# Optimization experiments

Measured on AMD Instinct MI355X. Metric: run time of the kernel, lower is better.

The kernel has to match this reference:

```python
import jax, jax.numpy as jnp
import numpy as np

B, T, HID = 8, 2048, 1024
NH, MD = 16, 16
UFC = 2  # len(use_for_context) = ['lr', 'rl']
MAT_EPS = 1e-5
VEC_EPS = 1e-6
SQRT_MD = float(np.sqrt(MD))


def setup_inputs() -> dict:
    key = jax.random.key(0)
    ks = jax.random.split(key, 5)
    s_in = 1.0 / np.sqrt(HID)
    s_out = 1.0 / np.sqrt(NH * MD * UFC)
    return {
        "hidden_states": jax.random.normal(ks[0], (B, T, HID), jnp.float32),
        "W_mat": jax.random.uniform(ks[1], (HID, NH * MD * MD), jnp.float32, -s_in, s_in),
        "b_mat": jax.random.uniform(ks[2], (NH * MD * MD,), jnp.float32, -s_in, s_in),
        "W_out": jax.random.uniform(ks[3], (NH * MD * UFC, HID), jnp.float32, -s_out, s_out),
        "b_out": jax.random.uniform(ks[4], (HID,), jnp.float32, -s_out, s_out),
    }


def _scan_vectors(m, v0, reverse):
    """Sequential matrix-vector recurrence with per-step L2 normalization.
    m: (T, B*NH, d, d); v0: (B*NH, d). Returns history (T, B*NH, d)
    (equal to torch history[1:] for lr, and reversed(history[1:]) for rl)."""
    def step(v, m_t):
        nv = jnp.einsum('bij,bj->bi', m_t, v)
        nv = nv / (jnp.linalg.norm(nv, axis=-1, keepdims=True) + VEC_EPS)
        return nv, nv
    _, hist = jax.lax.scan(step, v0, m, reverse=reverse)
    return hist


def reference(hidden_states, W_mat, b_mat, W_out, b_out):
    # predict_matrix: fc_to_mat + Frobenius matrix normalization ([-2,-1] branch)
    m = hidden_states @ W_mat + b_mat                       # (B, T, NH*MD*MD)
    m = m.reshape(B, T, NH, MD, MD).transpose(1, 0, 2, 3, 4)  # (T, B, NH, d, d)
    fro = jnp.linalg.norm(m, axis=(-2, -1), keepdims=True)
    m_norm = m / (fro + MAT_EPS) * SQRT_MD
    m_norm = m_norm.reshape(T, B * NH, MD, MD)

    # init_type == 'one': v[..., 0, :] = 1 -> e_0
    v0 = jnp.zeros((B * NH, MD), jnp.float32).at[:, 0].set(1.0)

    v_lr = _scan_vectors(m_norm, v0, reverse=False)  # (T, B*NH, d)
    v_rl = _scan_vectors(m_norm, v0, reverse=True)   # (T, B*NH, d)

    def to_bthd(v):
        return v.reshape(T, B, NH, MD).transpose(1, 0, 2, 3)  # (B, T, NH, d)

    x = jnp.concatenate([to_bthd(v_lr), to_bthd(v_rl)], axis=-1)  # (B, T, NH, 2d)
    # networks_for_heads == 'common': flatten heads, Linear, gelu (exact erf form)
    x = x.reshape(B, T, NH * MD * UFC) @ W_out + b_out
    return jax.nn.gelu(x, approximate=False)
```

## Files before the change

### kernel.cpp

```cpp
#include <hip/hip_runtime.h>
#include <math.h>

#define Tdim 2048
#define HIDd 1024
#define NHd 16
#define NCOL 4096
#define Cn 64
#define Ln 32
#define LSTR 40
#define KCAT 3072
#define KB 6144

typedef _Float16 f16x4  __attribute__((ext_vector_type(4)));
typedef _Float16 f16x8  __attribute__((ext_vector_type(8)));
typedef float    f32x4  __attribute__((ext_vector_type(4)));

typedef __attribute__((address_space(1))) void gvoid_t;
typedef __attribute__((address_space(3))) void lvoid_t;

__global__ __launch_bounds__(256) void conv_A_kernel(const float* __restrict__ hs,
                                                     _Float16* __restrict__ Ac)
{
    const size_t i = ((size_t)blockIdx.x * 256 + threadIdx.x) * 8;
    const size_t r = i >> 10, k = i & 1023;
    const float4 x0 = *(const float4*)(hs + i);
    const float4 x1 = *(const float4*)(hs + i + 4);
    const float v[8] = {x0.x, x0.y, x0.z, x0.w, x1.x, x1.y, x1.z, x1.w};
    f16x8 h, hm, l;
#pragma unroll
    for (int j = 0; j < 8; ++j) {
        const _Float16 hh = (_Float16)v[j];
        h[j]  = hh;
        hm[j] = (_Float16)(v[j] * 0.03125f);
        l[j]  = (_Float16)((v[j] - (float)hh) * 32.0f);
    }
    _Float16* o = Ac + r * KCAT + k;
    *(f16x8*)(o)        = h;
    *(f16x8*)(o + 1024) = hm;
    *(f16x8*)(o + 2048) = l;
}

__global__ __launch_bounds__(256) void conv_B_kernel(const float* __restrict__ W,
                                                     _Float16* __restrict__ Bc)
{
    __shared__ float t[32][33];
    const int tx = threadIdx.x & 31, ty = threadIdx.x >> 5;
    const int n0 = blockIdx.x * 32, k0 = blockIdx.y * 32;
#pragma unroll
    for (int i = 0; i < 4; ++i)
        t[ty + i * 8][tx] = W[(size_t)(k0 + ty + i * 8) * NCOL + n0 + tx];
    __syncthreads();
#pragma unroll
    for (int i = 0; i < 4; ++i) {
        const float w = t[tx][ty + i * 8];
        const _Float16 h = (_Float16)w;
        const size_t o = (size_t)(n0 + ty + i * 8) * KCAT + k0 + tx;
        Bc[o]        = h;
        Bc[o + 1024] = (_Float16)((w - (float)h) * 32.0f);
        Bc[o + 2048] = (_Float16)((float)h * 0.03125f);
    }
}

__global__ __launch_bounds__(256) void conv_W2T_kernel(const float* __restrict__ W,
                                                       _Float16* __restrict__ WT)
{
    __shared__ float t[32][33];
    const int tx = threadIdx.x & 31, ty = threadIdx.x >> 5;
    const int n0 = blockIdx.x * 32, k0 = blockIdx.y * 32;
#pragma unroll
    for (int i = 0; i < 4; ++i)
        t[ty + i * 8][tx] = W[(size_t)(k0 + ty + i * 8) * 1024 + n0 + tx];
    __syncthreads();
#pragma unroll
    for (int i = 0; i < 4; ++i)
        WT[(size_t)(n0 + ty + i * 8) * 512 + k0 + tx] = (_Float16)t[tx][ty + i * 8];
}

#define MFMA_PHASE(CPH) \
    _Pragma("unroll") \
    for (int m2_ = 0; m2_ < 2; ++m2_) { \
        _Pragma("unroll") \
        for (int nt_ = 0; nt_ < 4; ++nt_) { \
            acc[(CPH)*2 + m2_][nt_] = __builtin_amdgcn_mfma_f32_16x16x32_f16(af[m2_][0], bf[nt_][0], acc[(CPH)*2 + m2_][nt_], 0, 0, 0); \
            acc[(CPH)*2 + m2_][nt_] = __builtin_amdgcn_mfma_f32_16x16x32_f16(af[m2_][1], bf[nt_][1], acc[(CPH)*2 + m2_][nt_], 0, 0, 0); \
        } \
    }

#define PHASE(BUF, CPH, STAGE_EXPR, DOGATE) do { \
    af[0][0] = readA(BUF, (CPH)*2,     0); \
    af[0][1] = readA(BUF, (CPH)*2,     1); \
    af[1][0] = readA(BUF, (CPH)*2 + 1, 0); \
    af[1][1] = readA(BUF, (CPH)*2 + 1, 1); \
    if ((CPH) == 0) { \
        _Pragma("unroll") \
        for (int nt_ = 0; nt_ < 4; ++nt_) { bf[nt_][0] = readB(BUF, nt_, 0); bf[nt_][1] = readB(BUF, nt_, 1); } \
    } \
    STAGE_EXPR; \
    asm volatile("s_barrier" ::: "memory"); \
    asm volatile("s_waitcnt lgkmcnt(0)" ::: "memory"); \
    __builtin_amdgcn_sched_barrier(0); \
    __builtin_amdgcn_s_setprio(1); \
    MFMA_PHASE(CPH) \
    __builtin_amdgcn_s_setprio(0); \
    if (DOGATE) { \
        if (notlast) asm volatile("s_waitcnt vmcnt(6)" ::: "memory"); \
        else         asm volatile("s_waitcnt vmcnt(0)" ::: "memory"); \
    } \
    asm volatile("s_barrier" ::: "memory"); \
} while (0)

__global__ __launch_bounds__(512, 2) void gemm1_8ph(const _Float16* __restrict__ A,
                                                    const _Float16* __restrict__ B,
                                                    const float* __restrict__ bias,
                                                    float* __restrict__ Mout,
                                                    float* __restrict__ qout, int SS)
{
    __shared__ __align__(16) _Float16 sAB[4][256 * 64];
    const int tid = threadIdx.x;
    const int lane = tid & 63;
    const int wid = tid >> 6;
    const int wm = wid >> 2, wn = wid & 3;
    const int q = lane >> 4, ln = lane & 15;
    const int col0 = blockIdx.x * 256;
    const int row0 = blockIdx.y * 256;

    const char* Ab = (const char*)A + (size_t)row0 * KB;
    const char* Bb = (const char*)B + (size_t)col0 * KB;

    auto stage_chunk = [&](const char* g, int fr, int kt, char* ldsbase) {
        const int rr = tid >> 3;
        const int cb = (tid & 7) << 4;
        const char* src = g + (size_t)(fr + rr) * KB + (size_t)kt * 128 + (cb ^ ((rr & 7) << 4));
        char* dst = ldsbase + ((tid >> 6) << 10);
        __builtin_amdgcn_global_load_lds((gvoid_t*)src, (lvoid_t*)dst, 16, 0, 0);
    };
    auto stageA2g = [&](int b, int t, int h) {
        stage_chunk(Ab, h * 64,       t, (char*)&sAB[b][0] + (size_t)(h * 64) * 128);
        stage_chunk(Ab, 128 + h * 64, t, (char*)&sAB[b][0] + (size_t)(128 + h * 64) * 128);
    };
    auto stageB2 = [&](int b, int t, int h) {
        stage_chunk(Bb, h * 128,      t, (char*)&sAB[2 + b][0] + (size_t)(h * 128) * 128);
        stage_chunk(Bb, h * 128 + 64, t, (char*)&sAB[2 + b][0] + (size_t)(h * 128 + 64) * 128);
    };
    auto readA = [&](int b, int mf, int ks) -> f16x8 {
        const int r = wm * 128 + mf * 16 + ln;
        return *(const f16x8*)((const char*)&sAB[b][0] + r * 128 + ((ks * 64 + q * 16) ^ ((r & 7) << 4)));
    };
    auto readB = [&](int b, int nt, int ks) -> f16x8 {
        const int r = wn * 64 + nt * 16 + ln;
        return *(const f16x8*)((const char*)&sAB[2 + b][0] + r * 128 + ((ks * 64 + q * 16) ^ ((r & 7) << 4)));
    };

    stageB2(0, 0, 0); stageB2(0, 0, 1); stageA2g(0, 0, 0); stageA2g(0, 0, 1);
    stageB2(1, 1, 0); stageB2(1, 1, 1); stageA2g(1, 1, 0);

    f32x4 acc[8][4];
    const f32x4 z4 = {0.f, 0.f, 0.f, 0.f};
#pragma unroll
    for (int mf = 0; mf < 8; ++mf)
#pragma unroll
        for (int nt = 0; nt < 4; ++nt) acc[mf][nt] = z4;

    asm volatile("s_waitcnt vmcnt(6)" ::: "memory");
    asm volatile("s_barrier" ::: "memory");

    f16x8 af[2][2];
    f16x8 bf[4][2];

#pragma unroll 1
    for (int it = 0; it < 24; ++it) {
        const int t0 = it * 2;
        const bool notlast = (it != 23);
        PHASE(0, 0, (stageA2g(1, t0 + 1, 1)), 0);
        PHASE(0, 1, (notlast ? stageB2(0, t0 + 2, 0) : (void)0), 0);
        PHASE(0, 2, (notlast ? stageB2(0, t0 + 2, 1) : (void)0), 0);
        PHASE(0, 3, (notlast ? stageA2g(0, t0 + 2, 0) : (void)0), 1);
        PHASE(1, 0, (notlast ? stageA2g(0, t0 + 2, 1) : (void)0), 0);
        PHASE(1, 1, (notlast ? stageB2(1, t0 + 3, 0) : (void)0), 0);
        PHASE(1, 2, (notlast ? stageB2(1, t0 + 3, 1) : (void)0), 0);
        PHASE(1, 3, (notlast ? stageA2g(1, t0 + 3, 0) : (void)0), 1);
    }

    float* Mf = (float*)&sAB[0][0];
    const int seq = ((row0 >> 11) << 4) + blockIdx.x;
    const int cc   = wid & 3;
    const int dirw = wid >> 2;
    float bv[4];
#pragma unroll
    for (int nt = 0; nt < 4; ++nt) bv[nt] = bias[col0 + wn * 64 + nt * 16 + ln];

#pragma unroll 1
    for (int half = 0; half < 2; ++half) {
        __syncthreads();
        if (wm == half) {
#pragma unroll
            for (int mf = 0; mf < 8; ++mf)
#pragma unroll
                for (int nt = 0; nt < 4; ++nt)
#pragma unroll
                    for (int r = 0; r < 4; ++r)
                        Mf[(mf * 16 + q * 4 + r) * 256 + wn * 64 + nt * 16 + ln]
                            = acc[mf][nt][r] + bv[nt];
        }
        __syncthreads();

        const int cblk = half * 4 + cc;
        const int tb   = cblk * 32 - half * 128;
        float v[4];
#pragma unroll
        for (int r = 0; r < 4; ++r) v[r] = (q * 4 + r == ln) ? 1.0f : 0.0f;

        int tl = dirw ? (tb + 31) : tb;
        const int ds = dirw ? -1 : 1;
        float4 arow = *(const float4*)&Mf[tl * 256 + ln * 16 + q * 4];
        float f2 = arow.x*arow.x + arow.y*arow.y + arow.z*arow.z + arow.w*arow.w;
#pragma unroll
        for (int off = 1; off < 64; off <<= 1) f2 += __shfl_xor(f2, off);
        float sm = 4.0f * rsqrtf(f2 + 1e-12f);

        for (int s = 0; s < Ln; ++s) {
            const int tabs = (row0 & 2047) + (dirw ? (cblk * 32 + 31 - s) : (cblk * 32 + s));
            f16x4 mh, mlo;
            const float ar[4] = {arow.x * sm, arow.y * sm, arow.z * sm, arow.w * sm};
#pragma unroll
            for (int i = 0; i < 4; ++i) {
                const _Float16 h = (_Float16)ar[i];
                mh[i] = h; mlo[i] = (_Float16)((ar[i] - (float)h) * 1024.0f);
            }
            float smn = sm;
            if (s + 1 < Ln) {
                tl += ds;
                arow = *(const float4*)&Mf[tl * 256 + ln * 16 + q * 4];
                float f2n = arow.x*arow.x + arow.y*arow.y + arow.z*arow.z + arow.w*arow.w;
#pragma unroll
                for (int off = 1; off < 64; off <<= 1) f2n += __shfl_xor(f2n, off);
                smn = 4.0f * rsqrtf(f2n + 1e-12f);
            }
            f16x4 qh, ql;
#pragma unroll
            for (int r = 0; r < 4; ++r) {
                const _Float16 h = (_Float16)v[r];
                qh[r] = h; ql[r] = (_Float16)((v[r] - (float)h) * 1024.0f);
            }
            f32x4 a1 = {0.f,0.f,0.f,0.f}, a2 = {0.f,0.f,0.f,0.f};
            a1 = __builtin_amdgcn_mfma_f32_16x16x16f16(mh,  qh, a1, 0, 0, 0);
            a2 = __builtin_amdgcn_mfma_f32_16x16x16f16(mh,  ql, a2, 0, 0, 0);
            a2 = __builtin_amdgcn_mfma_f32_16x16x16f16(mlo, qh, a2, 0, 0, 0);
#pragma unroll
            for (int r = 0; r < 4; ++r) v[r] = a1[r] + a2[r] * (1.0f / 1024.0f);

            if (s & 1) {
                float mx = 0.f;
#pragma unroll
                for (int r = 0; r < 4; ++r) mx = fmaxf(mx, fabsf(v[r]));
#pragma unroll
                for (int off = 1; off < 64; off <<= 1) mx = fmaxf(mx, __shfl_xor(mx, off));
                const float inv = 1.0f / (mx + 1e-30f);
#pragma unroll
                for (int r = 0; r < 4; ++r) v[r] *= inv;
            }
            _Float16* Pp = (_Float16*)((char*)Mout
                         + ((size_t)seq * Tdim + tabs) * 1024 + dirw * 512);
#pragma unroll
            for (int r = 0; r < 4; ++r)
                Pp[(q * 4 + r) * 16 + ln] = (_Float16)v[r];
            sm = smn;
        }

        float ss = 0.f;
#pragma unroll
        for (int r = 0; r < 4; ++r) ss += v[r] * v[r];
#pragma unroll
        for (int off = 1; off < 64; off <<= 1) ss += __shfl_xor(ss, off);
        const float sl = 1.0f / (sqrtf(ss) + 1e-30f);
        const int cabs = ((row0 & 2047) >> 5) + cblk;
        float* qo = qout + ((size_t)(dirw * SS + seq) * Cn + cabs) * 256;
#pragma unroll
        for (int r = 0; r < 4; ++r)
            qo[(q * 4 + r) * 16 + ln] = v[r] * sl;
    }
}

__global__ __launch_bounds__(64) void stageB_kernel(const float* __restrict__ q,
                                                    float* __restrict__ vs, int SS)
{
    const int lane = threadIdx.x & 63;
    const int i = lane & 15;
    const int chain = blockIdx.x;
    const int dir = (chain >= SS) ? 1 : 0;
    const int seq = chain - dir * SS;
    const float* qb = q + (size_t)(dir * SS + seq) * Cn * 256;
    float* vb = vs + (size_t)(dir * SS + seq) * Cn * 16;

    float myw = (i == 0) ? 1.0f : 0.0f;
    float wv[16];
#pragma unroll
    for (int k2 = 0; k2 < 16; ++k2) wv[k2] = (k2 == 0) ? 1.0f : 0.0f;

    int cc = dir ? (Cn - 1) : 0;
    const float* Qp = qb + (size_t)cc * 256 + i * 16;
    float4 q0 = *(const float4*)(Qp + 0);
    float4 q1 = *(const float4*)(Qp + 4);
    float4 q2 = *(const float4*)(Qp + 8);
    float4 q3 = *(const float4*)(Qp + 12);

    for (int s = 0; s < Cn; ++s) {
        vb[cc * 16 + i] = myw;
        float nv = q0.x*wv[0] + q0.y*wv[1] + q0.z*wv[2] + q0.w*wv[3]
                 + q1.x*wv[4] + q1.y*wv[5] + q1.z*wv[6] + q1.w*wv[7]
                 + q2.x*wv[8] + q2.y*wv[9] + q2.z*wv[10] + q2.w*wv[11]
                 + q3.x*wv[12] + q3.y*wv[13] + q3.z*wv[14] + q3.w*wv[15];
        if (s + 1 < Cn) {
            const int ccn = dir ? (Cn - 2 - s) : (s + 1);
            const float* Qn = qb + (size_t)ccn * 256 + i * 16;
            q0 = *(const float4*)(Qn + 0);
            q1 = *(const float4*)(Qn + 4);
            q2 = *(const float4*)(Qn + 8);
            q3 = *(const float4*)(Qn + 12);
        }
        float s2 = nv * nv;
        s2 += __shfl_xor(s2, 1); s2 += __shfl_xor(s2, 2);
        s2 += __shfl_xor(s2, 4); s2 += __shfl_xor(s2, 8);
        const float wn = nv / (sqrtf(s2) + 1e-20f);
        myw = wn;
#pragma unroll
        for (int k2 = 0; k2 < 16; ++k2) wv[k2] = __shfl(wn, (lane & 48) | k2);
        cc = dir ? (Cn - 2 - s) : (s + 1);
    }
}

__global__ __launch_bounds__(256) void stageC2_kernel(const float* __restrict__ m,
                                                      const float* __restrict__ vs,
                                                      _Float16* __restrict__ x, int SS)
{
    const int tid = threadIdx.x;
    const int wave = tid >> 6, lane = tid & 63;
    const int dsc = blockIdx.x * 4 + wave;
    const int dirseq = dsc >> 6, c = dsc & (Cn - 1);
    const int dir = (dirseq >= SS) ? 1 : 0;
    const int seq = dirseq - dir * SS;
    const int bbl = seq >> 4, h = seq & 15;
    const _Float16* Pp = (const _Float16*)((const char*)m
                       + ((size_t)seq * Tdim + c * Ln) * 1024 + dir * 512);
    const float* vp = vs + (size_t)dsc * 16;

    float v[16];
#pragma unroll
    for (int k = 0; k < 16; ++k) v[k] = vp[k];

    const int tt = lane >> 4, j = lane & 15;
    const int t0 = c * Ln;
#pragma unroll
    for (int g = 0; g < 8; ++g) {
        const int s = g * 4 + tt;
        const _Float16* pr = Pp + (size_t)s * 512 + j * 16;
        const f16x8 p0 = *(const f16x8*)(pr);
        const f16x8 p1 = *(const f16x8*)(pr + 8);
        float nv = 0.f;
#pragma unroll
        for (int k = 0; k < 8; ++k) nv += (float)p0[k] * v[k];
#pragma unroll
        for (int k = 0; k < 8; ++k) nv += (float)p1[k] * v[k + 8];
        float s2 = nv * nv;
        s2 += __shfl_xor(s2, 1); s2 += __shfl_xor(s2, 2);
        s2 += __shfl_xor(s2, 4); s2 += __shfl_xor(s2, 8);
        const float vn = nv / (sqrtf(s2) + 1e-6f);
        const int t = t0 + s;
        x[(((size_t)bbl * Tdim + t) * NHd + h) * 32 + dir * 16 + j] = (_Float16)vn;
    }
}

__global__ __launch_bounds__(256) void gemm2_f16(const _Float16* __restrict__ A,
                                                 const _Float16* __restrict__ BT,
                                                 const float* __restrict__ bias,
                                                 float* __restrict__ out, int row0)
{
    __shared__ _Float16 Al[128 * LSTR];
    __shared__ _Float16 Bl[128 * LSTR];
    const int tid = threadIdx.x;
    const int wave = tid >> 6, lane = tid & 63;
    const int wm = wave & 1, wn = wave >> 1;
    const int qd = lane >> 4, ln = lane & 15;
    const int r0 = blockIdx.y * 128;
    const int c0 = blockIdx.x * 128;

    f32x4 acc[4][4] = {{{0.f,0.f,0.f,0.f}}};

    const int sr = tid >> 2, sc = tid & 3;
    const _Float16* Ag = A  + (size_t)(r0 + sr) * 512 + sc * 8;
    const _Float16* Bg = BT + (size_t)(c0 + sr) * 512 + sc * 8;
    _Float16* Alw = &Al[sr * LSTR + sc * 8];
    _Float16* Blw = &Bl[sr * LSTR + sc * 8];

    for (int k0 = 0; k0 < 512; k0 += 32) {
        const f16x8 a0 = *(const f16x8*)(Ag + k0);
        const f16x8 a1 = *(const f16x8*)(Ag + (size_t)64 * 512 + k0);
        const f16x8 b0 = *(const f16x8*)(Bg + k0);
        const f16x8 b1 = *(const f16x8*)(Bg + (size_t)64 * 512 + k0);
        __syncthreads();
        *(f16x8*)(Alw)             = a0;
        *(f16x8*)(Alw + 64 * LSTR) = a1;
        *(f16x8*)(Blw)             = b0;
        *(f16x8*)(Blw + 64 * LSTR) = b1;
        __syncthreads();
        f16x8 af[4], bfr[4];
#pragma unroll
        for (int mt = 0; mt < 4; ++mt)
            af[mt] = *(const f16x8*)&Al[(wm * 64 + mt * 16 + ln) * LSTR + qd * 8];
#pragma unroll
        for (int nt = 0; nt < 4; ++nt)
            bfr[nt] = *(const f16x8*)&Bl[(wn * 64 + nt * 16 + ln) * LSTR + qd * 8];
#pragma unroll
        for (int mt = 0; mt < 4; ++mt)
#pragma unroll
            for (int nt = 0; nt < 4; ++nt)
                acc[mt][nt] = __builtin_amdgcn_mfma_f32_16x16x32_f16(af[mt], bfr[nt], acc[mt][nt], 0, 0, 0);
    }
#pragma unroll
    for (int nt = 0; nt < 4; ++nt) {
        const int c = c0 + wn * 64 + nt * 16 + ln;
        const float bv = bias[c];
#pragma unroll
        for (int mt = 0; mt < 4; ++mt) {
#pragma unroll
            for (int r = 0; r < 4; ++r) {
                const int row = r0 + wm * 64 + mt * 16 + qd * 4 + r;
                float v = acc[mt][nt][r] + bv;
                v = 0.5f * v * (1.0f + erff(v * 0.70710678118654752f));
                out[(size_t)(row0 + row) * 1024 + c] = v;
            }
        }
    }
}

extern "C" void kernel_launch(void* const* d_in, const int* in_sizes, int n_in,
                              void* d_out, int out_size, void* d_ws, size_t ws_size,
                              hipStream_t stream)
{
    const float* hs    = (const float*)d_in[0];
    const float* W_mat = (const float*)d_in[1];
    const float* b_mat = (const float*)d_in[2];
    const float* W_out = (const float*)d_in[3];
    const float* b_out = (const float*)d_in[4];
    float* out = (float*)d_out;

    const size_t per_bb = (32ull << 20) + (2ull << 20) + (12ull << 20) + (128ull << 10);
    const size_t wbase  = 25ull << 20;
    int nbb = 8;
    while (nbb > 1 && ws_size < wbase + (size_t)nbb * per_bb) nbb >>= 1;

    char* base = (char*)d_ws;
    _Float16* W2T = (_Float16*)base;
    _Float16* Bc  = (_Float16*)(base + (1ull << 20));
    size_t off = wbase;
    float* m  = (float*)(base + off);  off += (size_t)nbb * (32ull << 20);
    float* qx = (float*)(base + off);  off += (size_t)nbb * (2ull << 20);
    _Float16* Ac = (_Float16*)(base + off); off += (size_t)nbb * (12ull << 20);
    float* vs = (float*)(base + off);

    conv_B_kernel<<<dim3(128, 32), 256, 0, stream>>>(W_mat, Bc);
    conv_W2T_kernel<<<dim3(32, 16), 256, 0, stream>>>(W_out, W2T);

    for (int bb0 = 0; bb0 < 8; bb0 += nbb) {
        const int row0 = bb0 * Tdim;
        const int SS = nbb * 16;
        conv_A_kernel<<<nbb * 1024, 256, 0, stream>>>(hs + (size_t)row0 * HIDd, Ac);
        gemm1_8ph<<<dim3(16, nbb * 8), 512, 0, stream>>>(Ac, Bc, b_mat, m, qx, SS);
        stageB_kernel<<<2 * SS, 64, 0, stream>>>(qx, vs, SS);
        stageC2_kernel<<<SS * Cn / 2, 256, 0, stream>>>(m, vs, (_Float16*)qx, SS);
        gemm2_f16<<<dim3(8, nbb * 16), 256, 0, stream>>>((_Float16*)qx, W2T, b_out, out, row0);
    }
}
```

Measured before the change: 786.3 us.

## Replace output GEMM with 8-phase pipelined global_load_lds kernel and swizzle Mf stores

Rewrites the second GEMM as a 256x256-tile, 512-thread kernel that stages A and B directly into LDS with global_load_lds, using XOR-swizzled layouts and a double-buffered phase schedule reused from the first GEMM. This aims to overlap global loads with MFMA work and cut LDS bank conflicts and per-iteration barriers. It also XOR-swizzles the Mf scratch layout in the scan stage to reduce bank conflicts on the row reads. The larger tiles mean fewer blocks (4x8 per batch chunk), which may lower occupancy and wave balance.

```diff
diff --git a/kernel.cpp b/kernel.cpp
--- a/kernel.cpp
+++ b/kernel.cpp
@@ -7,9 +7,9 @@
 #define NCOL 4096
 #define Cn 64
 #define Ln 32
-#define LSTR 40
 #define KCAT 3072
 #define KB 6144
+#define KB2 1024
 
 typedef _Float16 f16x4  __attribute__((ext_vector_type(4)));
 typedef _Float16 f16x8  __attribute__((ext_vector_type(8)));
@@ -198,9 +198,11 @@
 #pragma unroll
                 for (int nt = 0; nt < 4; ++nt)
 #pragma unroll
-                    for (int r = 0; r < 4; ++r)
-                        Mf[(mf * 16 + q * 4 + r) * 256 + wn * 64 + nt * 16 + ln]
-                            = acc[mf][nt][r] + bv[nt];
+                    for (int r = 0; r < 4; ++r) {
+                        const int mrow = mf * 16 + q * 4 + r;
+                        const int mcol = (wn * 64 + nt * 16 + ln) ^ ((mrow & 4) << 2);
+                        Mf[mrow * 256 + mcol] = acc[mf][nt][r] + bv[nt];
+                    }
         }
         __syncthreads();
 
@@ -212,7 +214,7 @@
 
         int tl = dirw ? (tb + 31) : tb;
         const int ds = dirw ? -1 : 1;
-        float4 arow = *(const float4*)&Mf[tl * 256 + ln * 16 + q * 4];
+        float4 arow = *(const float4*)&Mf[tl * 256 + ((ln * 16 + q * 4) ^ ((tl & 4) << 2))];
         float f2 = arow.x*arow.x + arow.y*arow.y + arow.z*arow.z + arow.w*arow.w;
 #pragma unroll
         for (int off = 1; off < 64; off <<= 1) f2 += __shfl_xor(f2, off);
@@ -230,7 +232,7 @@
             float smn = sm;
             if (s + 1 < Ln) {
                 tl += ds;
-                arow = *(const float4*)&Mf[tl * 256 + ln * 16 + q * 4];
+                arow = *(const float4*)&Mf[tl * 256 + ((ln * 16 + q * 4) ^ ((tl & 4) << 2))];
                 float f2n = arow.x*arow.x + arow.y*arow.y + arow.z*arow.z + arow.w*arow.w;
 #pragma unroll
                 for (int off = 1; off < 64; off <<= 1) f2n += __shfl_xor(f2n, off);
@@ -370,64 +372,89 @@
     }
 }
 
-__global__ __launch_bounds__(256) void gemm2_f16(const _Float16* __restrict__ A,
-                                                 const _Float16* __restrict__ BT,
-                                                 const float* __restrict__ bias,
-                                                 float* __restrict__ out, int row0)
-{
-    __shared__ _Float16 Al[128 * LSTR];
-    __shared__ _Float16 Bl[128 * LSTR];
+__global__ __launch_bounds__(512, 2) void gemm2_8ph(const _Float16* __restrict__ A,
+                                                    const _Float16* __restrict__ BT,
+                                                    const float* __restrict__ bias,
+                                                    float* __restrict__ out, int row0p)
+{
+    __shared__ __align__(16) _Float16 sAB[4][256 * 64];
     const int tid = threadIdx.x;
-    const int wave = tid >> 6, lane = tid & 63;
-    const int wm = wave & 1, wn = wave >> 1;
-    const int qd = lane >> 4, ln = lane & 15;
-    const int r0 = blockIdx.y * 128;
-    const int c0 = blockIdx.x * 128;
-
-    f32x4 acc[4][4] = {{{0.f,0.f,0.f,0.f}}};
-
-    const int sr = tid >> 2, sc = tid & 3;
-    const _Float16* Ag = A  + (size_t)(r0 + sr) * 512 + sc * 8;
-    const _Float16* Bg = BT + (size_t)(c0 + sr) * 512 + sc * 8;
-    _Float16* Alw = &Al[sr * LSTR + sc * 8];
-    _Float16* Blw = &Bl[sr * LSTR + sc * 8];
-
-    for (int k0 = 0; k0 < 512; k0 += 32) {
-        const f16x8 a0 = *(const f16x8*)(Ag + k0);
-        const f16x8 a1 = *(const f16x8*)(Ag + (size_t)64 * 512 + k0);
-        const f16x8 b0 = *(const f16x8*)(Bg + k0);
-        const f16x8 b1 = *(const f16x8*)(Bg + (size_t)64 * 512 + k0);
-        __syncthreads();
-        *(f16x8*)(Alw)             = a0;
-        *(f16x8*)(Alw + 64 * LSTR) = a1;
-        *(f16x8*)(Blw)             = b0;
-        *(f16x8*)(Blw + 64 * LSTR) = b1;
-        __syncthreads();
-        f16x8 af[4], bfr[4];
-#pragma unroll
-        for (int mt = 0; mt < 4; ++mt)
-            af[mt] = *(const f16x8*)&Al[(wm * 64 + mt * 16 + ln) * LSTR + qd * 8];
-#pragma unroll
-        for (int nt = 0; nt < 4; ++nt)
-            bfr[nt] = *(const f16x8*)&Bl[(wn * 64 + nt * 16 + ln) * LSTR + qd * 8];
-#pragma unroll
-        for (int mt = 0; mt < 4; ++mt)
-#pragma unroll
-            for (int nt = 0; nt < 4; ++nt)
-                acc[mt][nt] = __builtin_amdgcn_mfma_f32_16x16x32_f16(af[mt], bfr[nt], acc[mt][nt], 0, 0, 0);
-    }
+    const int lane = tid & 63;
+    const int wid = tid >> 6;
+    const int wm = wid >> 2, wn = wid & 3;
+    const int q = lane >> 4, ln = lane & 15;
+    const int col0 = blockIdx.x * 256;
+    const int row0 = blockIdx.y * 256;
+
+    const char* Ab = (const char*)A  + (size_t)row0 * KB2;
+    const char* Bb = (const char*)BT + (size_t)col0 * KB2;
+
+    auto stage_chunk = [&](const char* g, int fr, int kt, char* ldsbase) {
+        const int rr = tid >> 3;
+        const int cb = (tid & 7) << 4;
+        const char* src = g + (size_t)(fr + rr) * KB2 + (size_t)kt * 128 + (cb ^ ((rr & 7) << 4));
+        char* dst = ldsbase + ((tid >> 6) << 10);
+        __builtin_amdgcn_global_load_lds((gvoid_t*)src, (lvoid_t*)dst, 16, 0, 0);
+    };
+    auto stageA2g = [&](int b, int t, int h) {
+        stage_chunk(Ab, h * 64,       t, (char*)&sAB[b][0] + (size_t)(h * 64) * 128);
+        stage_chunk(Ab, 128 + h * 64, t, (char*)&sAB[b][0] + (size_t)(128 + h * 64) * 128);
+    };
+    auto stageB2 = [&](int b, int t, int h) {
+        stage_chunk(Bb, h * 128,      t, (char*)&sAB[2 + b][0] + (size_t)(h * 128) * 128);
+        stage_chunk(Bb, h * 128 + 64, t, (char*)&sAB[2 + b][0] + (size_t)(h * 128 + 64) * 128);
+    };
+    auto readA = [&](int b, int mf, int ks) -> f16x8 {
+        const int r = wm * 128 + mf * 16 + ln;
+        return *(const f16x8*)((const char*)&sAB[b][0] + r * 128 + ((ks * 64 + q * 16) ^ ((r & 7) << 4)));
+    };
+    auto readB = [&](int b, int nt, int ks) -> f16x8 {
+        const int r = wn * 64 + nt * 16 + ln;
+        return *(const f16x8*)((const char*)&sAB[2 + b][0] + r * 128 + ((ks * 64 + q * 16) ^ ((r & 7) << 4)));
+    };
+
+    stageB2(0, 0, 0); stageB2(0, 0, 1); stageA2g(0, 0, 0); stageA2g(0, 0, 1);
+    stageB2(1, 1, 0); stageB2(1, 1, 1); stageA2g(1, 1, 0);
+
+    f32x4 acc[8][4];
+    const f32x4 z4 = {0.f, 0.f, 0.f, 0.f};
+#pragma unroll
+    for (int mf = 0; mf < 8; ++mf)
+#pragma unroll
+        for (int nt = 0; nt < 4; ++nt) acc[mf][nt] = z4;
+
+    asm volatile("s_waitcnt vmcnt(6)" ::: "memory");
+    asm volatile("s_barrier" ::: "memory");
+
+    f16x8 af[2][2];
+    f16x8 bf[4][2];
+
+#pragma unroll 1
+    for (int it = 0; it < 4; ++it) {
+        const int t0 = it * 2;
+        const bool notlast = (it != 3);
+        PHASE(0, 0, (stageA2g(1, t0 + 1, 1)), 0);
+        PHASE(0, 1, (notlast ? stageB2(0, t0 + 2, 0) : (void)0), 0);
+        PHASE(0, 2, (notlast ? stageB2(0, t0 + 2, 1) : (void)0), 0);
+        PHASE(0, 3, (notlast ? stageA2g(0, t0 + 2, 0) : (void)0), 1);
+        PHASE(1, 0, (notlast ? stageA2g(0, t0 + 2, 1) : (void)0), 0);
+        PHASE(1, 1, (notlast ? stageB2(1, t0 + 3, 0) : (void)0), 0);
+        PHASE(1, 2, (notlast ? stageB2(1, t0 + 3, 1) : (void)0), 0);
+        PHASE(1, 3, (notlast ? stageA2g(1, t0 + 3, 0) : (void)0), 1);
+    }
+
 #pragma unroll
     for (int nt = 0; nt < 4; ++nt) {
-        const int c = c0 + wn * 64 + nt * 16 + ln;
+        const int c = col0 + wn * 64 + nt * 16 + ln;
         const float bv = bias[c];
 #pragma unroll
-        for (int mt = 0; mt < 4; ++mt) {
+        for (int mf = 0; mf < 8; ++mf) {
 #pragma unroll
             for (int r = 0; r < 4; ++r) {
-                const int row = r0 + wm * 64 + mt * 16 + qd * 4 + r;
-                float v = acc[mt][nt][r] + bv;
+                const int row = row0 + wm * 128 + mf * 16 + q * 4 + r;
+                float v = acc[mf][nt][r] + bv;
                 v = 0.5f * v * (1.0f + erff(v * 0.70710678118654752f));
-                out[(size_t)(row0 + row) * 1024 + c] = v;
+                out[(size_t)(row0p + row) * 1024 + c] = v;
             }
         }
     }
@@ -468,6 +495,6 @@
         gemm1_8ph<<<dim3(16, nbb * 8), 512, 0, stream>>>(Ac, Bc, b_mat, m, qx, SS);
         stageB_kernel<<<2 * SS, 64, 0, stream>>>(qx, vs, SS);
         stageC2_kernel<<<SS * Cn / 2, 256, 0, stream>>>(m, vs, (_Float16*)qx, SS);
-        gemm2_f16<<<dim3(8, nbb * 16), 256, 0, stream>>>((_Float16*)qx, W2T, b_out, out, row0);
-    }
-}
+        gemm2_8ph<<<dim3(4, nbb * 8), 512, 0, stream>>>((_Float16*)qx, W2T, b_out, out, row0);
+    }
+}
```

After: 797.4 us. No clear change (+1.4%).
